# Kernel optimization log

Hardware: AMD Instinct MI355X
Metric: run time of the kernel (lower is better)

Reference implementation:

```python
import jax, jax.numpy as jnp
import numpy as np
from jax import lax

N_GROUPS = 2
TOPK_GROUPS = 1
TOPK = 4
ROUTE_SCALE = 1.0


def setup_inputs() -> dict:
    key = jax.random.key(0)
    k1, k2 = jax.random.split(key)
    T, D, E = 524288, 256, 64
    x = jax.random.normal(k1, (T, D), dtype=jnp.float32)
    W = jax.random.normal(k2, (E, D), dtype=jnp.float32) * 0.02  # router weight [out, in]
    return {"x": x, "W": W}


def reference(x, W):
    T = x.shape[0]
    E = W.shape[0]
    logits = x @ W.T  # [T, E]
    scores = jax.nn.softmax(logits.astype(jnp.float32), axis=-1)
    original_scores = scores
    # grouped masking (bias is None -> amax group score)
    g = scores.reshape(T, N_GROUPS, E // N_GROUPS)
    group_scores = g.max(axis=-1)  # [T, G]
    _, gidx = lax.top_k(group_scores, TOPK_GROUPS)  # [T, topk_groups]
    keep = jnp.zeros((T, N_GROUPS), dtype=bool).at[jnp.arange(T)[:, None], gidx].set(True)
    masked = jnp.where(keep[:, :, None], g, -jnp.inf).reshape(T, E)
    _, indices = lax.top_k(masked, TOPK)  # [T, topk]
    weights = jnp.take_along_axis(original_scores, indices, axis=1)
    weights = weights * ROUTE_SCALE
    return weights.astype(x.dtype), indices
```

## Files before the change

kernel.cpp:

```cpp
#include <hip/hip_runtime.h>
#include <hip/hip_bf16.h>
#include <stdint.h>


typedef __attribute__((ext_vector_type(8))) short bf16x8;
typedef __attribute__((ext_vector_type(4))) float f32x4;
typedef __attribute__((ext_vector_type(4))) int i32x4;

#define SPLIT_OFF 1024
#define LIST_OFF 102400
#define DELTA 5e-5f

__device__ __forceinline__ f32x4 mf(const i32x4& a, const i32x4& b,
                                    const f32x4& c) {
  return __builtin_amdgcn_mfma_f32_16x16x32_bf16(
      __builtin_bit_cast(bf16x8, a), __builtin_bit_cast(bf16x8, b), c, 0, 0, 0);
}

__device__ __forceinline__ int packhi(unsigned e0, unsigned e1) {
  return (int)__builtin_amdgcn_perm(e1, e0, 0x07060302u);
}

__global__ void zero_meta(int* meta) { meta[0] = 0; }

__global__ void split_w(const float* __restrict__ W,
                        unsigned short* __restrict__ ws, int n) {
  int i = blockIdx.x * 256 + threadIdx.x;
  if (i >= n) return;
  float w = W[i];
  unsigned u = __float_as_uint(w);
  unsigned uh = u & 0xFFFF0000u;
  float rf = w - __uint_as_float(uh);
  unsigned short lv[2];
  lv[0] = (unsigned short)(uh >> 16);
  lv[1] = (unsigned short)(__float_as_uint(rf) >> 16);
  int e = i >> 8, k = i & 255;
  int nt = e >> 4, le = e & 15;
  int c = k >> 5, lg = (k >> 3) & 3, kk = k & 7;
  int lane = lg * 16 + le;
#pragma unroll
  for (int v = 0; v < 2; ++v)
    ws[(((c * 8 + v * 4 + nt) * 64) + lane) * 8 + kk] = lv[v];
}

struct XF { i32x4 h, m, l; };

__device__ __forceinline__ XF split_x(f32x4 a, f32x4 b) {
  float xs[8] = {a[0], a[1], a[2], a[3], b[0], b[1], b[2], b[3]};
  unsigned hu[8], mu[8], lu[8];
#pragma unroll
  for (int j = 0; j < 8; ++j) {
    unsigned u = __float_as_uint(xs[j]);
    unsigned uh = u & 0xFFFF0000u;
    float r = xs[j] - __uint_as_float(uh);
    unsigned um = __float_as_uint(r) & 0xFFFF0000u;
    float lf = r - __uint_as_float(um);
    hu[j] = u;
    mu[j] = __float_as_uint(r);
    lu[j] = __float_as_uint(lf);
  }
  XF f;
#pragma unroll
  for (int wd = 0; wd < 4; ++wd) {
    f.h[wd] = packhi(hu[2 * wd], hu[2 * wd + 1]);
    f.m[wd] = packhi(mu[2 * wd], mu[2 * wd + 1]);
    f.l[wd] = packhi(lu[2 * wd], lu[2 * wd + 1]);
  }
  return f;
}

#define GL(dst, ptr, OFFSTR)                                       \
  asm volatile("global_load_dwordx4 %0, %1, off offset:" OFFSTR    \
               : "=v"(dst)                                         \
               : "v"(ptr))

#define WAITV(NSTR)                                         \
  do {                                                      \
    asm volatile("s_waitcnt vmcnt(" NSTR ")" ::: "memory"); \
    __builtin_amdgcn_sched_barrier(0);                      \
  } while (0)

__global__ __launch_bounds__(256, 2) void gate_kernel(
    const float* __restrict__ x, const unsigned short* __restrict__ wsp,
    float* __restrict__ out, int* __restrict__ meta, int* __restrict__ list,
    int cap, int T) {
  const int t = threadIdx.x;
  const int lane = t & 63;
  const int wid = t >> 6;
  const int le = lane & 15;
  const int lg = lane >> 4;
  const int tokbase = blockIdx.x * 128 + wid * 32;

  const float* xa0 = x + (size_t)(tokbase + le) * 256 + lg * 8;
  const float* xa1 = xa0 + 16 * 256;
  const char* wl = (const char*)wsp + lane * 16;

  f32x4 xbuf[3][4];
  i32x4 wbuf[2][8];
  f32x4 acc[4][2];
#pragma unroll
  for (int nt = 0; nt < 4; ++nt)
#pragma unroll
    for (int tt = 0; tt < 2; ++tt) acc[nt][tt] = (f32x4)0.0f;

#define STAGE_X(c)                                   \
  do {                                               \
    const float* p0_ = xa0 + (c) * 32;               \
    const float* p1_ = xa1 + (c) * 32;               \
    GL(xbuf[(c) % 3][0], p0_, "0");                  \
    GL(xbuf[(c) % 3][1], p0_, "16");                 \
    GL(xbuf[(c) % 3][2], p1_, "0");                  \
    GL(xbuf[(c) % 3][3], p1_, "16");                 \
  } while (0)

#define STAGE_W(c)                                   \
  do {                                               \
    const char* pA_ = wl + (c) * 8192;               \
    const char* pB_ = pA_ + 4096;                    \
    GL(wbuf[(c) & 1][0], pA_, "0");                  \
    GL(wbuf[(c) & 1][1], pA_, "1024");               \
    GL(wbuf[(c) & 1][2], pA_, "2048");               \
    GL(wbuf[(c) & 1][3], pA_, "3072");               \
    GL(wbuf[(c) & 1][4], pB_, "0");                  \
    GL(wbuf[(c) & 1][5], pB_, "1024");               \
    GL(wbuf[(c) & 1][6], pB_, "2048");               \
    GL(wbuf[(c) & 1][7], pB_, "3072");               \
  } while (0)

#define COMP(c)                                           \
  do {                                                    \
    XF b0 = split_x(xbuf[(c) % 3][0], xbuf[(c) % 3][1]);  \
    XF b1 = split_x(xbuf[(c) % 3][2], xbuf[(c) % 3][3]);  \
    _Pragma("unroll") for (int nt = 0; nt < 4; ++nt) {    \
      const i32x4 ah = wbuf[(c) & 1][nt];                 \
      const i32x4 am = wbuf[(c) & 1][4 + nt];             \
      acc[nt][0] = mf(ah, b0.h, acc[nt][0]);              \
      acc[nt][0] = mf(ah, b0.m, acc[nt][0]);              \
      acc[nt][0] = mf(am, b0.h, acc[nt][0]);              \
      acc[nt][0] = mf(am, b0.m, acc[nt][0]);              \
      acc[nt][0] = mf(ah, b0.l, acc[nt][0]);              \
      acc[nt][1] = mf(ah, b1.h, acc[nt][1]);              \
      acc[nt][1] = mf(ah, b1.m, acc[nt][1]);              \
      acc[nt][1] = mf(am, b1.h, acc[nt][1]);              \
      acc[nt][1] = mf(am, b1.m, acc[nt][1]);              \
      acc[nt][1] = mf(ah, b1.l, acc[nt][1]);              \
    }                                                     \
  } while (0)

  STAGE_X(0);
  STAGE_X(1);
  STAGE_W(0);
  STAGE_W(1); STAGE_X(2); WAITV("12"); COMP(0);
  STAGE_W(2); STAGE_X(3); WAITV("16"); COMP(1);
  STAGE_W(3); STAGE_X(4); WAITV("16"); COMP(2);
  STAGE_W(4); STAGE_X(5); WAITV("16"); COMP(3);
  STAGE_W(5); STAGE_X(6); WAITV("16"); COMP(4);
  STAGE_W(6); STAGE_X(7); WAITV("16"); COMP(5);
  STAGE_W(7); WAITV("12"); COMP(6);
  WAITV("0"); COMP(7);

#pragma unroll
  for (int tt = 0; tt < 2; ++tt) {
    float l[16];
#pragma unroll
    for (int nt = 0; nt < 4; ++nt)
#pragma unroll
      for (int j = 0; j < 4; ++j) l[nt * 4 + j] = acc[nt][tt][j];

    float g0 = l[0], g1 = l[8];
#pragma unroll
    for (int j = 1; j < 8; ++j) {
      g0 = fmaxf(g0, l[j]);
      g1 = fmaxf(g1, l[8 + j]);
    }
    g0 = fmaxf(g0, __shfl_xor(g0, 16));
    g0 = fmaxf(g0, __shfl_xor(g0, 32));
    g1 = fmaxf(g1, __shfl_xor(g1, 16));
    g1 = fmaxf(g1, __shfl_xor(g1, 32));
    const int g = (g1 > g0) ? 1 : 0;
    const float m = fmaxf(g0, g1);

    float sum = 0.f;
#pragma unroll
    for (int k = 0; k < 16; ++k) sum += __expf(l[k] - m);
    sum += __shfl_xor(sum, 16);
    sum += __shfl_xor(sum, 32);
    const float inv = 1.0f / sum;

    float c[8];
    int ce[8];
#pragma unroll
    for (int j2 = 0; j2 < 8; ++j2) {
      c[j2] = l[g * 8 + j2];
      ce[j2] = (2 * g + (j2 >> 2)) * 16 + 4 * lg + (j2 & 3);
    }

    float v5[5];
    int e5[5];
#pragma unroll
    for (int it = 0; it < 5; ++it) {
      float bv = c[0];
      int be = ce[0];
#pragma unroll
      for (int j2 = 1; j2 < 8; ++j2) {
        bool gt = c[j2] > bv;
        bv = gt ? c[j2] : bv;
        be = gt ? ce[j2] : be;
      }
#pragma unroll
      for (int st = 0; st < 2; ++st) {
        int msk = 16 << st;
        float ov = __shfl_xor(bv, msk);
        int oe = __shfl_xor(be, msk);
        bool tk = (ov > bv) || (ov == bv && oe < be);
        bv = tk ? ov : bv;
        be = tk ? oe : be;
      }
      v5[it] = bv;
      e5[it] = be;
#pragma unroll
      for (int j2 = 0; j2 < 8; ++j2)
        c[j2] = (ce[j2] == be) ? -3.0e38f : c[j2];
    }

    float ming = fabsf(g0 - g1);
#pragma unroll
    for (int it = 0; it < 4; ++it) ming = fminf(ming, v5[it] - v5[it + 1]);

    if (lg == 0) {
      size_t trow = (size_t)tokbase + tt * 16 + le;
      *(float4*)&out[trow * 4] =
          make_float4(__expf(v5[0] - m) * inv, __expf(v5[1] - m) * inv,
                      __expf(v5[2] - m) * inv, __expf(v5[3] - m) * inv);
      *(float4*)&out[(size_t)T * 4 + trow * 4] = make_float4(
          (float)e5[0], (float)e5[1], (float)e5[2], (float)e5[3]);
      if (ming < DELTA) {
        int p = atomicAdd(meta, 1);
        if (p < cap) list[p] = (int)trow;
      }
    }
  }
}

__global__ __launch_bounds__(64) void fix_kernel(
    const float* __restrict__ x, const float* __restrict__ W,
    float* __restrict__ out, const int* __restrict__ meta,
    const int* __restrict__ list, int cap, int T) {
  const int e = threadIdx.x;
  int cnt = meta[0];
  cnt = cnt < cap ? cnt : cap;
  for (int i = blockIdx.x; i < cnt; i += gridDim.x) {
    const int tok = list[i];
    const float* xr = x + (size_t)tok * 256;
    const float* wr = W + (size_t)e * 256;
    float acc = 0.f;
#pragma unroll 8
    for (int d = 0; d < 256; d += 4) {
      float4 xv = *(const float4*)(xr + d);
      float4 wv = *(const float4*)(wr + d);
      acc = fmaf(xv.x, wv.x, acc);
      acc = fmaf(xv.y, wv.y, acc);
      acc = fmaf(xv.z, wv.z, acc);
      acc = fmaf(xv.w, wv.w, acc);
    }
    float gm = acc;
#pragma unroll
    for (int st = 0; st < 5; ++st) gm = fmaxf(gm, __shfl_xor(gm, 1 << st));
    float om = __shfl_xor(gm, 32);
    float g0 = (e < 32) ? gm : om;
    float g1 = (e < 32) ? om : gm;
    const int g = (g1 > g0) ? 1 : 0;
    const float m = fmaxf(g0, g1);
    float sum = __expf(acc - m);
#pragma unroll
    for (int st = 0; st < 6; ++st) sum += __shfl_xor(sum, 1 << st);
    const float inv = 1.0f / sum;

    float cand = ((e >> 5) == g) ? acc : -3.0e38f;
    float w4[4], i4[4];
#pragma unroll
    for (int it = 0; it < 4; ++it) {
      float bv = cand;
      int be = e;
#pragma unroll
      for (int st = 0; st < 6; ++st) {
        int msk = 1 << st;
        float ov = __shfl_xor(bv, msk);
        int oe = __shfl_xor(be, msk);
        bool tk = (ov > bv) || (ov == bv && oe < be);
        bv = tk ? ov : bv;
        be = tk ? oe : be;
      }
      w4[it] = __expf(bv - m) * inv;
      i4[it] = (float)be;
      if (e == be) cand = -3.0e38f;
    }
    if (e == 0) {
      *(float4*)&out[(size_t)tok * 4] = make_float4(w4[0], w4[1], w4[2], w4[3]);
      *(float4*)&out[(size_t)T * 4 + (size_t)tok * 4] =
          make_float4(i4[0], i4[1], i4[2], i4[3]);
    }
  }
}

extern "C" void kernel_launch(void* const* d_in, const int* in_sizes, int n_in,
                              void* d_out, int out_size, void* d_ws,
                              size_t ws_size, hipStream_t stream) {
  const float* x = (const float*)d_in[0];
  const float* W = (const float*)d_in[1];
  float* out = (float*)d_out;
  int T = in_sizes[0] / 256;
  int nW = in_sizes[1];
  int* meta = (int*)d_ws;
  unsigned short* wsp = (unsigned short*)((char*)d_ws + SPLIT_OFF);
  int* list = (int*)((char*)d_ws + LIST_OFF);
  int cap = (ws_size > LIST_OFF + 4) ? (int)((ws_size - LIST_OFF) / 4) : 0;
  hipLaunchKernelGGL(zero_meta, dim3(1), dim3(1), 0, stream, meta);
  hipLaunchKernelGGL(split_w, dim3((nW + 255) / 256), dim3(256), 0, stream, W,
                     wsp, nW);
  hipLaunchKernelGGL(gate_kernel, dim3(T / 128), dim3(256), 0, stream, x, wsp,
                     out, meta, list, cap, T);
  hipLaunchKernelGGL(fix_kernel, dim3(1024), dim3(64), 0, stream, x, W, out,
                     meta, list, cap, T);
}
```

Measured before the change: 167.6 us.

## Stage split weights in LDS, double tokens per wave, drop low x term

Each block now copies the pre-split bf16 weight table into shared memory once with global_load_lds, and waves read it from LDS instead of streaming it from global memory every chunk. Each wave handles 64 tokens instead of 32, which halves the grid and spreads the weight traffic over more compute. The third (low) x split term is removed, cutting MFMAs per tile from 5 to 4. To cover the larger approximation error, the near-tie threshold DELTA is doubled and the fix-up kernel gets more blocks, which risks more tokens going down the slow recheck path.

```diff
diff --git a/kernel.cpp b/kernel.cpp
--- a/kernel.cpp
+++ b/kernel.cpp
@@ -9,7 +9,7 @@
 
 #define SPLIT_OFF 1024
 #define LIST_OFF 102400
-#define DELTA 5e-5f
+#define DELTA 1e-4f
 
 __device__ __forceinline__ f32x4 mf(const i32x4& a, const i32x4& b,
                                     const f32x4& c) {
@@ -19,6 +19,12 @@
 
 __device__ __forceinline__ int packhi(unsigned e0, unsigned e1) {
   return (int)__builtin_amdgcn_perm(e1, e0, 0x07060302u);
+}
+
+__device__ __forceinline__ void gload16(const void* g, void* l) {
+  __builtin_amdgcn_global_load_lds(
+      (const __attribute__((address_space(1))) void*)g,
+      (__attribute__((address_space(3))) void*)l, 16, 0, 0);
 }
 
 __global__ void zero_meta(int* meta) { meta[0] = 0; }
@@ -43,35 +49,26 @@
     ws[(((c * 8 + v * 4 + nt) * 64) + lane) * 8 + kk] = lv[v];
 }
 
-struct XF { i32x4 h, m, l; };
-
-__device__ __forceinline__ XF split_x(f32x4 a, f32x4 b) {
+struct XF2 { i32x4 h, m; };
+
+__device__ __forceinline__ XF2 split2(f32x4 a, f32x4 b) {
   float xs[8] = {a[0], a[1], a[2], a[3], b[0], b[1], b[2], b[3]};
-  unsigned hu[8], mu[8], lu[8];
-#pragma unroll
-  for (int j = 0; j < 8; ++j) {
-    unsigned u = __float_as_uint(xs[j]);
-    unsigned uh = u & 0xFFFF0000u;
-    float r = xs[j] - __uint_as_float(uh);
-    unsigned um = __float_as_uint(r) & 0xFFFF0000u;
-    float lf = r - __uint_as_float(um);
-    hu[j] = u;
-    mu[j] = __float_as_uint(r);
-    lu[j] = __float_as_uint(lf);
-  }
-  XF f;
+  XF2 f;
 #pragma unroll
   for (int wd = 0; wd < 4; ++wd) {
-    f.h[wd] = packhi(hu[2 * wd], hu[2 * wd + 1]);
-    f.m[wd] = packhi(mu[2 * wd], mu[2 * wd + 1]);
-    f.l[wd] = packhi(lu[2 * wd], lu[2 * wd + 1]);
+    unsigned u0 = __float_as_uint(xs[2 * wd]);
+    unsigned u1 = __float_as_uint(xs[2 * wd + 1]);
+    f.h[wd] = packhi(u0, u1);
+    float r0 = xs[2 * wd] - __uint_as_float(u0 & 0xFFFF0000u);
+    float r1 = xs[2 * wd + 1] - __uint_as_float(u1 & 0xFFFF0000u);
+    f.m[wd] = packhi(__float_as_uint(r0), __float_as_uint(r1));
   }
   return f;
 }
 
-#define GL(dst, ptr, OFFSTR)                                       \
-  asm volatile("global_load_dwordx4 %0, %1, off offset:" OFFSTR    \
-               : "=v"(dst)                                         \
+#define GL(dst, ptr, OFFSTR)                                    \
+  asm volatile("global_load_dwordx4 %0, %1, off offset:" OFFSTR \
+               : "=v"(dst)                                      \
                : "v"(ptr))
 
 #define WAITV(NSTR)                                         \
@@ -84,83 +81,76 @@
     const float* __restrict__ x, const unsigned short* __restrict__ wsp,
     float* __restrict__ out, int* __restrict__ meta, int* __restrict__ list,
     int cap, int T) {
+  __shared__ i32x4 WL[4096];
+
   const int t = threadIdx.x;
   const int lane = t & 63;
   const int wid = t >> 6;
   const int le = lane & 15;
   const int lg = lane >> 4;
-  const int tokbase = blockIdx.x * 128 + wid * 32;
-
-  const float* xa0 = x + (size_t)(tokbase + le) * 256 + lg * 8;
-  const float* xa1 = xa0 + 16 * 256;
-  const char* wl = (const char*)wsp + lane * 16;
-
-  f32x4 xbuf[3][4];
-  i32x4 wbuf[2][8];
-  f32x4 acc[4][2];
+  const int tokbase = blockIdx.x * 256 + wid * 64;
+
+  {
+    const char* wsrc = (const char*)wsp + t * 16;
+    char* wdst = (char*)WL + t * 16;
+#pragma unroll
+    for (int i = 0; i < 16; ++i) gload16(wsrc + i * 4096, wdst + i * 4096);
+  }
+  WAITV("0");
+  __syncthreads();
+
+  const float* xa[4];
+#pragma unroll
+  for (int t4 = 0; t4 < 4; ++t4)
+    xa[t4] = x + (size_t)(tokbase + t4 * 16 + le) * 256 + lg * 8;
+
+  f32x4 xbuf[3][8];
+  f32x4 acc[4][4];
 #pragma unroll
   for (int nt = 0; nt < 4; ++nt)
 #pragma unroll
-    for (int tt = 0; tt < 2; ++tt) acc[nt][tt] = (f32x4)0.0f;
+    for (int t4 = 0; t4 < 4; ++t4) acc[nt][t4] = (f32x4)0.0f;
 
 #define STAGE_X(c)                                   \
   do {                                               \
-    const float* p0_ = xa0 + (c) * 32;               \
-    const float* p1_ = xa1 + (c) * 32;               \
-    GL(xbuf[(c) % 3][0], p0_, "0");                  \
-    GL(xbuf[(c) % 3][1], p0_, "16");                 \
-    GL(xbuf[(c) % 3][2], p1_, "0");                  \
-    GL(xbuf[(c) % 3][3], p1_, "16");                 \
+    _Pragma("unroll") for (int t4 = 0; t4 < 4; ++t4) { \
+      const float* p_ = xa[t4] + (c) * 32;           \
+      GL(xbuf[(c) % 3][2 * t4], p_, "0");            \
+      GL(xbuf[(c) % 3][2 * t4 + 1], p_, "16");       \
+    }                                                \
   } while (0)
 
-#define STAGE_W(c)                                   \
-  do {                                               \
-    const char* pA_ = wl + (c) * 8192;               \
-    const char* pB_ = pA_ + 4096;                    \
-    GL(wbuf[(c) & 1][0], pA_, "0");                  \
-    GL(wbuf[(c) & 1][1], pA_, "1024");               \
-    GL(wbuf[(c) & 1][2], pA_, "2048");               \
-    GL(wbuf[(c) & 1][3], pA_, "3072");               \
-    GL(wbuf[(c) & 1][4], pB_, "0");                  \
-    GL(wbuf[(c) & 1][5], pB_, "1024");               \
-    GL(wbuf[(c) & 1][6], pB_, "2048");               \
-    GL(wbuf[(c) & 1][7], pB_, "3072");               \
-  } while (0)
-
-#define COMP(c)                                           \
-  do {                                                    \
-    XF b0 = split_x(xbuf[(c) % 3][0], xbuf[(c) % 3][1]);  \
-    XF b1 = split_x(xbuf[(c) % 3][2], xbuf[(c) % 3][3]);  \
-    _Pragma("unroll") for (int nt = 0; nt < 4; ++nt) {    \
-      const i32x4 ah = wbuf[(c) & 1][nt];                 \
-      const i32x4 am = wbuf[(c) & 1][4 + nt];             \
-      acc[nt][0] = mf(ah, b0.h, acc[nt][0]);              \
-      acc[nt][0] = mf(ah, b0.m, acc[nt][0]);              \
-      acc[nt][0] = mf(am, b0.h, acc[nt][0]);              \
-      acc[nt][0] = mf(am, b0.m, acc[nt][0]);              \
-      acc[nt][0] = mf(ah, b0.l, acc[nt][0]);              \
-      acc[nt][1] = mf(ah, b1.h, acc[nt][1]);              \
-      acc[nt][1] = mf(ah, b1.m, acc[nt][1]);              \
-      acc[nt][1] = mf(am, b1.h, acc[nt][1]);              \
-      acc[nt][1] = mf(am, b1.m, acc[nt][1]);              \
-      acc[nt][1] = mf(ah, b1.l, acc[nt][1]);              \
-    }                                                     \
-  } while (0)
+#define ITER(c, NSTR)                                             \
+  {                                                               \
+    if ((c) < 6) STAGE_X((c) + 2);                                \
+    i32x4 wr[8];                                                  \
+    _Pragma("unroll") for (int q = 0; q < 8; ++q)                 \
+        wr[q] = WL[(((c) * 8 + q) << 6) + lane];                  \
+    WAITV(NSTR);                                                  \
+    _Pragma("unroll") for (int t4 = 0; t4 < 4; ++t4) {            \
+      XF2 b = split2(xbuf[(c) % 3][2 * t4], xbuf[(c) % 3][2 * t4 + 1]); \
+      _Pragma("unroll") for (int nt = 0; nt < 4; ++nt) {          \
+        acc[nt][t4] = mf(wr[nt], b.h, acc[nt][t4]);               \
+        acc[nt][t4] = mf(wr[nt], b.m, acc[nt][t4]);               \
+        acc[nt][t4] = mf(wr[4 + nt], b.h, acc[nt][t4]);           \
+        acc[nt][t4] = mf(wr[4 + nt], b.m, acc[nt][t4]);           \
+      }                                                           \
+    }                                                             \
+  }
 
   STAGE_X(0);
   STAGE_X(1);
-  STAGE_W(0);
-  STAGE_W(1); STAGE_X(2); WAITV("12"); COMP(0);
-  STAGE_W(2); STAGE_X(3); WAITV("16"); COMP(1);
-  STAGE_W(3); STAGE_X(4); WAITV("16"); COMP(2);
-  STAGE_W(4); STAGE_X(5); WAITV("16"); COMP(3);
-  STAGE_W(5); STAGE_X(6); WAITV("16"); COMP(4);
-  STAGE_W(6); STAGE_X(7); WAITV("16"); COMP(5);
-  STAGE_W(7); WAITV("12"); COMP(6);
-  WAITV("0"); COMP(7);
-
-#pragma unroll
-  for (int tt = 0; tt < 2; ++tt) {
+  ITER(0, "16");
+  ITER(1, "16");
+  ITER(2, "16");
+  ITER(3, "16");
+  ITER(4, "16");
+  ITER(5, "16");
+  ITER(6, "8");
+  ITER(7, "0");
+
+#pragma unroll
+  for (int tt = 0; tt < 4; ++tt) {
     float l[16];
 #pragma unroll
     for (int nt = 0; nt < 4; ++nt)
@@ -318,8 +308,8 @@
   hipLaunchKernelGGL(zero_meta, dim3(1), dim3(1), 0, stream, meta);
   hipLaunchKernelGGL(split_w, dim3((nW + 255) / 256), dim3(256), 0, stream, W,
                      wsp, nW);
-  hipLaunchKernelGGL(gate_kernel, dim3(T / 128), dim3(256), 0, stream, x, wsp,
+  hipLaunchKernelGGL(gate_kernel, dim3(T / 256), dim3(256), 0, stream, x, wsp,
                      out, meta, list, cap, T);
-  hipLaunchKernelGGL(fix_kernel, dim3(1024), dim3(64), 0, stream, x, W, out,
+  hipLaunchKernelGGL(fix_kernel, dim3(2048), dim3(64), 0, stream, x, W, out,
                      meta, list, cap, T);
 }
```

Result: faster. 148.1 us (-11.6%).
